# Kernel tuning notes

Hardware: AMD Instinct MI355X
Metric: run time of the kernel (lower is better)

Reference implementation:

```python
import jax, jax.numpy as jnp
import numpy as np


def _rnn_scan(x_pre, W_hh, b_hh, h0):
    # x_pre: [S, B, H] precomputed input projection; returns stacked h: [S, B, H]
    def step(h, xp):
        h = jnp.tanh(xp + h @ W_hh.T + b_hh)
        return h, h
    _, hs = jax.lax.scan(step, h0, x_pre)
    return hs


def setup_inputs() -> dict:
    key = jax.random.key(0)
    ks = jax.random.split(key, 12)
    B, S, E, H, V = 16, 256, 512, 1024, 32000
    sE, sH = 1.0 / np.sqrt(E), 1.0 / np.sqrt(H)
    return {
        "x_ids": jax.random.randint(ks[0], (B, S), 0, V),
        "emb": jax.random.normal(ks[1], (V, E), jnp.float32),
        "W_ih1": jax.random.normal(ks[2], (H, E), jnp.float32) * sE,
        "b_ih1": jax.random.normal(ks[3], (H,), jnp.float32) * sH,
        "W_hh1": jax.random.normal(ks[4], (H, H), jnp.float32) * sH,
        "b_hh1": jax.random.normal(ks[5], (H,), jnp.float32) * sH,
        "W_ih2": jax.random.normal(ks[6], (H, H), jnp.float32) * sH,
        "b_ih2": jax.random.normal(ks[7], (H,), jnp.float32) * sH,
        "W_hh2": jax.random.normal(ks[8], (H, H), jnp.float32) * sH,
        "b_hh2": jax.random.normal(ks[9], (H,), jnp.float32) * sH,
        "W_fc": jax.random.normal(ks[10], (V, H), jnp.float32) * sH,
        "b_fc": jax.random.normal(ks[11], (V,), jnp.float32) * sH,
    }


def reference(x_ids, emb, W_ih1, b_ih1, W_hh1, b_hh1, W_ih2, b_ih2, W_hh2, b_hh2, W_fc, b_fc):
    B, S = x_ids.shape
    H = W_hh1.shape[0]
    x = emb[x_ids]  # [B, S, E]
    # layer 1: precompute input projection for all steps, scan over time
    x1 = jnp.einsum('bse,he->sbh', x, W_ih1) + b_ih1  # [S, B, H]
    h0 = jnp.zeros((B, H), x.dtype)
    h1s = _rnn_scan(x1, W_hh1, b_hh1, h0)  # [S, B, H]
    # layer 2
    x2 = jnp.einsum('sbh,gh->sbg', h1s, W_ih2) + b_ih2
    h2s = _rnn_scan(x2, W_hh2, b_hh2, h0)  # [S, B, H]
    # per-step fc + softmax, vectorized
    logits = jnp.einsum('sbh,vh->bsv', h2s, W_fc) + b_fc  # [B, S, V]
    return jax.nn.softmax(logits, axis=-1)
```

## Files before the change

kernel.cpp:

```cpp
#include <hip/hip_runtime.h>
#include <cstdint>
#include <cstddef>
#include <math.h>

typedef unsigned short u16;
typedef __attribute__((ext_vector_type(4))) float f32x4;
typedef __attribute__((ext_vector_type(8))) short s16x8;
typedef __attribute__((ext_vector_type(8))) unsigned short u16x8;
typedef __attribute__((ext_vector_type(4))) unsigned short u16x4;
typedef __attribute__((ext_vector_type(4))) unsigned u32x4;

#define B_ 16
#define S_ 256
#define E_ 512
#define H_ 1024
#define V_ 32000
#define M_TOK (S_*B_)
#define BH (B_*H_)
#define NT_FC 250
#define MT_FC 32
#define NCVT 250

__device__ __forceinline__ u16 f2bf(float f) {
  union { float f; unsigned u; } x; x.f = f;
  unsigned r = x.u + 0x7fffu + ((x.u >> 16) & 1u);
  return (u16)(r >> 16);
}
__device__ __forceinline__ float bf2f(u16 x) {
  union { unsigned u; float f; } c; c.u = ((unsigned)x) << 16; return c.f;
}

__device__ __forceinline__ void sc_load16(s16x8& d, const u16* p) {
  asm volatile("global_load_dwordx4 %0, %1, off sc0 sc1" : "=v"(d) : "v"(p));
}
__device__ __forceinline__ void sc_load16u(u32x4& d, const u16* p) {
  asm volatile("global_load_dwordx4 %0, %1, off sc0 sc1" : "=v"(d) : "v"(p));
}
__device__ __forceinline__ void sc_load8w(u16x4& d, const u16* p) {
  asm volatile("global_load_dwordx2 %0, %1, off sc0 sc1\n\ts_waitcnt vmcnt(0)"
               : "=v"(d) : "v"(p) : "memory");
}
__device__ __forceinline__ int sc_load4w(const int* p) {
  int d;
  asm volatile("global_load_dword %0, %1, off sc0 sc1\n\ts_waitcnt vmcnt(0)"
               : "=v"(d) : "v"(p) : "memory");
  return d;
}
__device__ __forceinline__ void sc_store8(u16* p, u16x4 v) {
  asm volatile("global_store_dwordx2 %0, %1, off sc0 sc1" :: "v"(p), "v"(v) : "memory");
}
__device__ __forceinline__ void sc_store4(int* p, int v) {
  asm volatile("global_store_dword %0, %1, off sc0 sc1" :: "v"(p), "v"(v) : "memory");
}
__device__ __forceinline__ void wait_vm0() {
  asm volatile("s_waitcnt vmcnt(0)" ::: "memory");
}

__global__ __launch_bounds__(256)
void k_cvt_small(const float* s0, u16* d0, int n0,
                 const float* s1, u16* d1, int n1,
                 const float* s2, u16* d2, int n2,
                 const float* s3, u16* d3, int n3)
{
  const int total = n0 + n1 + n2 + n3;
  for (int i = blockIdx.x*256 + threadIdx.x; i < total; i += gridDim.x*256) {
    const float* s; u16* d; int j = i;
    if (j < n0) { s = s0; d = d0; }
    else { j -= n0;
      if (j < n1) { s = s1; d = d1; }
      else { j -= n1;
        if (j < n2) { s = s2; d = d2; }
        else { j -= n2; s = s3; d = d3; } } }
    float4 v = reinterpret_cast<const float4*>(s)[j];
    ushort4 o;
    o.x = f2bf(v.x); o.y = f2bf(v.y); o.z = f2bf(v.z); o.w = f2bf(v.w);
    reinterpret_cast<ushort4*>(d)[j] = o;
  }
}

__global__ __launch_bounds__(256) void k_embed(const int* __restrict__ ids,
                                               const float* __restrict__ emb,
                                               u16* __restrict__ A1) {
  int g = blockIdx.x*256 + threadIdx.x;
  int m = g >> 6;
  int c = g & 63;
  int s = m >> 4, b = m & 15;
  int id = ids[b*S_ + s];
  const float4* src = reinterpret_cast<const float4*>(emb + (size_t)id*E_ + (size_t)c*8);
  float4 v0 = src[0], v1 = src[1];
  u16x8 o;
  o[0]=f2bf(v0.x); o[1]=f2bf(v0.y); o[2]=f2bf(v0.z); o[3]=f2bf(v0.w);
  o[4]=f2bf(v1.x); o[5]=f2bf(v1.y); o[6]=f2bf(v1.z); o[7]=f2bf(v1.w);
  *reinterpret_cast<u16x8*>(A1 + (size_t)m*E_ + (size_t)c*8) = o;
}

#define BM 128
#define BN 128
#define BK 32

__device__ __forceinline__ void gload_lds16(const u16* g, u16* l) {
  __builtin_amdgcn_global_load_lds(
      (const __attribute__((address_space(1))) void*)g,
      (__attribute__((address_space(3))) void*)l,
      16, 0, 0);
}

template<int FCMODE>
__global__ __launch_bounds__(256)
void k_gemm(const u16* __restrict__ A, const u16* __restrict__ Bw,
            float* __restrict__ C, const float* __restrict__ bias,
            int M, int N, int K)
{
  __shared__ u16 lA[2][BM*BK];
  __shared__ u16 lB[2][BN*BK];
  const int tid = threadIdx.x;
  const int l = tid & 63, w = tid >> 6;

  const int nwg = gridDim.x * gridDim.y;
  int d = blockIdx.y * gridDim.x + blockIdx.x;
  int tt = (d & 7) * (nwg >> 3) + (d >> 3);
  const int n0 = (tt / gridDim.y) * BN;
  const int m0 = (tt % gridDim.y) * BM;

  const int wr = w >> 1, wc = w & 1;

  const int L0 = (w*2+0)*64 + l;
  const int L1 = (w*2+1)*64 + l;
  const int r0 = L0 >> 2, r1 = L1 >> 2;
  const int c0 = (L0 & 3) ^ ((r0 >> 1) & 3);
  const int c1 = (L1 & 3) ^ ((r1 >> 1) & 3);
  const u16* gA0 = A  + (size_t)(m0 + r0)*K + c0*8;
  const u16* gA1 = A  + (size_t)(m0 + r1)*K + c1*8;
  const u16* gB0 = Bw + (size_t)(n0 + r0)*K + c0*8;
  const u16* gB1 = Bw + (size_t)(n0 + r1)*K + c1*8;

  const int fr = l & 15;
  const int xc = (l >> 4) ^ ((fr >> 1) & 3);
  int aoff[4], boff[4];
#pragma unroll
  for (int f = 0; f < 4; ++f) {
    aoff[f] = (wr*64 + f*16 + fr) * BK + xc*8;
    boff[f] = (wc*64 + f*16 + fr) * BK + xc*8;
  }

  f32x4 acc[4][4] = {};
  const int KT = K / BK;

  gload_lds16(gA0, &lA[0][(w*2+0)*512]);
  gload_lds16(gA1, &lA[0][(w*2+1)*512]);
  gload_lds16(gB0, &lB[0][(w*2+0)*512]);
  gload_lds16(gB1, &lB[0][(w*2+1)*512]);
  __syncthreads();

  for (int kt = 0; kt < KT; ++kt) {
    const int buf = kt & 1;
    if (kt + 1 < KT) {
      const int koff = (kt+1)*BK;
      gload_lds16(gA0 + koff, &lA[buf^1][(w*2+0)*512]);
      gload_lds16(gA1 + koff, &lA[buf^1][(w*2+1)*512]);
      gload_lds16(gB0 + koff, &lB[buf^1][(w*2+0)*512]);
      gload_lds16(gB1 + koff, &lB[buf^1][(w*2+1)*512]);
    }
    s16x8 af[4], bq[4];
#pragma unroll
    for (int f = 0; f < 4; ++f) af[f] = *reinterpret_cast<const s16x8*>(&lA[buf][aoff[f]]);
#pragma unroll
    for (int f = 0; f < 4; ++f) bq[f] = *reinterpret_cast<const s16x8*>(&lB[buf][boff[f]]);
#pragma unroll
    for (int fm = 0; fm < 4; ++fm)
#pragma unroll
      for (int fn = 0; fn < 4; ++fn)
        acc[fm][fn] = __builtin_amdgcn_mfma_f32_16x16x32_bf16(af[fm], bq[fn], acc[fm][fn], 0, 0, 0);
    __syncthreads();
  }

  const int rowb = (l >> 4) * 4;
  const int colb = l & 15;
#pragma unroll
  for (int fm = 0; fm < 4; ++fm) {
#pragma unroll
    for (int fn = 0; fn < 4; ++fn) {
      const int col = n0 + wc*64 + fn*16 + colb;
#pragma unroll
      for (int r = 0; r < 4; ++r) {
        const int row = m0 + wr*64 + fm*16 + rowb + r;
        float v = acc[fm][fn][r];
        if (FCMODE == 2) {
          ((u16*)C)[(size_t)row*N + col] = f2bf(v);
        } else {
          C[(size_t)row*N + col] = v;
        }
      }
    }
  }
}

__device__ __forceinline__ void fc_tile(const u16* __restrict__ A, const u16* __restrict__ Bw,
                                        float* __restrict__ C, const float* __restrict__ bias,
                                        float* __restrict__ stat,
                                        int m0, int n0, u16* smem)
{
  const int tid = threadIdx.x;
  const int l = tid & 63, w = tid >> 6;
  const int wr = w >> 1, wc = w & 1;
  const int nt = n0 / BN;
  u16* lA = smem;
  u16* lB = smem + 8192;

  const int L0 = (w*2+0)*64 + l;
  const int L1 = (w*2+1)*64 + l;
  const int r0 = L0 >> 2, r1 = L1 >> 2;
  const int c0 = (L0 & 3) ^ ((r0 >> 1) & 3);
  const int c1 = (L1 & 3) ^ ((r1 >> 1) & 3);
  const u16* gA0 = A  + (size_t)(m0 + r0)*H_ + c0*8;
  const u16* gA1 = A  + (size_t)(m0 + r1)*H_ + c1*8;
  const u16* gB0 = Bw + (size_t)(n0 + r0)*H_ + c0*8;
  const u16* gB1 = Bw + (size_t)(n0 + r1)*H_ + c1*8;

  const int fr = l & 15;
  const int xc = (l >> 4) ^ ((fr >> 1) & 3);
  int aoff[4], boff[4];
#pragma unroll
  for (int f = 0; f < 4; ++f) {
    aoff[f] = (wr*64 + f*16 + fr) * BK + xc*8;
    boff[f] = (wc*64 + f*16 + fr) * BK + xc*8;
  }

  f32x4 acc[4][4] = {};

  gload_lds16(gA0, lA + (w*2+0)*512);
  gload_lds16(gA1, lA + (w*2+1)*512);
  gload_lds16(gB0, lB + (w*2+0)*512);
  gload_lds16(gB1, lB + (w*2+1)*512);
  __syncthreads();

  for (int kt = 0; kt < 32; ++kt) {
    const int buf = kt & 1;
    if (kt + 1 < 32) {
      const int koff = (kt+1)*BK;
      gload_lds16(gA0 + koff, lA + (buf^1)*4096 + (w*2+0)*512);
      gload_lds16(gA1 + koff, lA + (buf^1)*4096 + (w*2+1)*512);
      gload_lds16(gB0 + koff, lB + (buf^1)*4096 + (w*2+0)*512);
      gload_lds16(gB1 + koff, lB + (buf^1)*4096 + (w*2+1)*512);
    }
    s16x8 af[4], bq[4];
#pragma unroll
    for (int f = 0; f < 4; ++f) af[f] = *reinterpret_cast<const s16x8*>(lA + buf*4096 + aoff[f]);
#pragma unroll
    for (int f = 0; f < 4; ++f) bq[f] = *reinterpret_cast<const s16x8*>(lB + buf*4096 + boff[f]);
#pragma unroll
    for (int fm = 0; fm < 4; ++fm)
#pragma unroll
      for (int fn = 0; fn < 4; ++fn)
        acc[fm][fn] = __builtin_amdgcn_mfma_f32_16x16x32_bf16(af[fm], bq[fn], acc[fm][fn], 0, 0, 0);
    __syncthreads();
  }

  const int rowb = (l >> 4) * 4;
  const int colb = l & 15;

#pragma unroll
  for (int fm = 0; fm < 4; ++fm) {
#pragma unroll
    for (int fn = 0; fn < 4; ++fn) {
      const int col = n0 + wc*64 + fn*16 + colb;
      const float bv = bias[col];
#pragma unroll
      for (int r = 0; r < 4; ++r) {
        const int row = m0 + wr*64 + fm*16 + rowb + r;
        const int b = row & 15, s = row >> 4;
        acc[fm][fn][r] += bv;
        C[((size_t)(b*S_ + s))*V_ + col] = acc[fm][fn][r];
      }
    }
  }

  float* stats = reinterpret_cast<float*>(smem);
#pragma unroll
  for (int fm = 0; fm < 4; ++fm) {
#pragma unroll
    for (int r = 0; r < 4; ++r) {
      float sm = __expf(acc[fm][0][r]) + __expf(acc[fm][1][r])
               + __expf(acc[fm][2][r]) + __expf(acc[fm][3][r]);
#pragma unroll
      for (int o = 1; o <= 8; o <<= 1) sm += __shfl_xor(sm, o);
      if (colb == 0) {
        const int j = wr*64 + fm*16 + rowb + r;
        stats[j*2 + wc] = sm;
      }
    }
  }
  __syncthreads();
  if (tid < 128) {
    stat[(size_t)(m0 + tid)*NT_FC + nt] = stats[tid*2 + 0] + stats[tid*2 + 1];
  }
}

__global__ __launch_bounds__(256)
void k_mega(const u16* __restrict__ Whh1, const u16* __restrict__ Wih2,
            const u16* __restrict__ Whh2, const u16* __restrict__ x1b,
            const float* __restrict__ bih1, const float* __restrict__ bhh1,
            const float* __restrict__ bih2, const float* __restrict__ bhh2,
            u16* __restrict__ h1s, u16* __restrict__ u2s, u16* __restrict__ h2s,
            int* __restrict__ s1, int* __restrict__ su, int* __restrict__ s2,
            const float* __restrict__ Wfc, u16* __restrict__ Wfcb,
            const float* __restrict__ bfc,
            float* __restrict__ out, float* __restrict__ stat,
            int* __restrict__ prog2, int* __restrict__ done, int* __restrict__ cvtdone)
{
  __shared__ u16 smem[16384];
  const int bid = blockIdx.x;
  const int tid = threadIdx.x;

  if (bid < 48) {
    const int l = tid & 63, w = tid >> 6;
    const int role = bid >> 4;
    const int blk  = bid & 15;
    const int rowA = blk*64 + w*16 + (l & 15);
    const int kc = l >> 4;
    const int bcol = l & 15;
    const int i0 = blk*64 + w*16 + kc*4;
    const int jme = (tid & 127) >> 3;

    const u16* Wsel = (role == 0) ? Whh1 : (role == 1) ? Wih2 : Whh2;
    s16x8 wf[32];
    {
      const u16* wp = Wsel + (size_t)rowA*H_ + kc*8;
#pragma unroll
      for (int ks = 0; ks < 32; ++ks) wf[ks] = *reinterpret_cast<const s16x8*>(wp + ks*32);
    }

    auto stage = [&](const u16* src, const int* sentrow) {
      while (sc_load4w(sentrow + jme) != 0) __builtin_amdgcn_s_sleep(2);
      s16x8 stg[8];
#pragma unroll
      for (int r = 0; r < 8; ++r) sc_load16(stg[r], src + (size_t)(tid + r*256)*8);
      wait_vm0();
#pragma unroll
      for (int r = 0; r < 8; ++r) {
        int idx8 = tid + r*256;
        int bt = idx8 >> 7, c8 = idx8 & 127;
        *reinterpret_cast<s16x8*>(reinterpret_cast<char*>(smem) +
            bt*2048 + ((c8*16) ^ ((bt & 7) << 4))) = stg[r];
      }
    };

    const int swz = (bcol & 7) << 4;
    auto hfrag = [&](int ks) -> s16x8 {
      return *reinterpret_cast<const s16x8*>(
          reinterpret_cast<const char*>(smem) + bcol*2048 + (((kc*16) + ks*64) ^ swz));
    };
    auto mfma32 = [&](f32x4& a0, f32x4& a1, f32x4& a2, f32x4& a3) {
#pragma unroll
      for (int ks = 0; ks < 32; ks += 4) {
        a0 = __builtin_amdgcn_mfma_f32_16x16x32_bf16(wf[ks+0], hfrag(ks+0), a0, 0, 0, 0);
        a1 = __builtin_amdgcn_mfma_f32_16x16x32_bf16(wf[ks+1], hfrag(ks+1), a1, 0, 0, 0);
        a2 = __builtin_amdgcn_mfma_f32_16x16x32_bf16(wf[ks+2], hfrag(ks+2), a2, 0, 0, 0);
        a3 = __builtin_amdgcn_mfma_f32_16x16x32_bf16(wf[ks+3], hfrag(ks+3), a3, 0, 0, 0);
      }
    };

    if (role == 0) {
      float bc[4];
#pragma unroll
      for (int r = 0; r < 4; ++r) bc[r] = bih1[i0+r] + bhh1[i0+r];
      for (int t = 0; t < S_; ++t) {
        f32x4 a0 = {}, a1 = {}, a2 = {}, a3 = {};
        if (t > 0) {
          stage(h1s + (size_t)(t-1)*BH, s1 + (t-1)*16);
          __syncthreads();
          mfma32(a0, a1, a2, a3);
        }
        u16x4 xr = *reinterpret_cast<const u16x4*>(x1b + (size_t)(t*B_ + bcol)*H_ + i0);
        f32x4 tot = (a0 + a1) + (a2 + a3);
        u16x4 o;
        o[0] = f2bf(tanhf(tot[0] + bf2f(xr[0]) + bc[0]));
        o[1] = f2bf(tanhf(tot[1] + bf2f(xr[1]) + bc[1]));
        o[2] = f2bf(tanhf(tot[2] + bf2f(xr[2]) + bc[2]));
        o[3] = f2bf(tanhf(tot[3] + bf2f(xr[3]) + bc[3]));
        sc_store8(h1s + (size_t)(t*B_ + bcol)*H_ + i0, o);
        wait_vm0();
        __syncthreads();
        if (tid == 0) sc_store4(s1 + t*16 + blk, 0);
      }
    } else if (role == 1) {
      float bc[4];
#pragma unroll
      for (int r = 0; r < 4; ++r) bc[r] = bih2[i0+r] + bhh2[i0+r];
      for (int t = 0; t < S_; ++t) {
        stage(h1s + (size_t)t*BH, s1 + t*16);
        __syncthreads();
        f32x4 a0 = {}, a1 = {}, a2 = {}, a3 = {};
        mfma32(a0, a1, a2, a3);
        f32x4 tot = (a0 + a1) + (a2 + a3);
        u16x4 o;
        o[0] = f2bf(tot[0] + bc[0]);
        o[1] = f2bf(tot[1] + bc[1]);
        o[2] = f2bf(tot[2] + bc[2]);
        o[3] = f2bf(tot[3] + bc[3]);
        sc_store8(u2s + (size_t)(t*B_ + bcol)*H_ + i0, o);
        wait_vm0();
        __syncthreads();
        if (tid == 0) sc_store4(su + t*16 + blk, 0);
      }
    } else {
      for (int t = 0; t < S_; ++t) {
        if (tid == 0) {
          while (sc_load4w(su + t*16 + blk) != 0) __builtin_amdgcn_s_sleep(2);
        }
        if (t > 0) stage(h2s + (size_t)(t-1)*BH, s2 + (t-1)*16);
        __syncthreads();
        u16x4 uv;
        sc_load8w(uv, u2s + (size_t)(t*B_ + bcol)*H_ + i0);
        f32x4 a0 = {}, a1 = {}, a2 = {}, a3 = {};
        if (t > 0) mfma32(a0, a1, a2, a3);
        f32x4 tot = (a0 + a1) + (a2 + a3);
        u16x4 o;
        o[0] = f2bf(tanhf(tot[0] + bf2f(uv[0])));
        o[1] = f2bf(tanhf(tot[1] + bf2f(uv[1])));
        o[2] = f2bf(tanhf(tot[2] + bf2f(uv[2])));
        o[3] = f2bf(tanhf(tot[3] + bf2f(uv[3])));
        sc_store8(h2s + (size_t)(t*B_ + bcol)*H_ + i0, o);
        wait_vm0();
        __syncthreads();
        if (tid == 0) {
          sc_store4(s2 + t*16 + blk, 0);
          sc_store4(prog2 + blk, t + 1);
        }
      }
    }
    return;
  }

  if (bid < 48 + NCVT) {
    const int nt = bid - 48;
    const float* src = Wfc  + (size_t)nt*128*H_;
    u16*         dst = Wfcb + (size_t)nt*128*H_;
#pragma unroll 4
    for (int i = 0; i < 128; ++i) {
      const int idx = tid + i*256;
      float4 v = reinterpret_cast<const float4*>(src)[idx];
      u16x4 o;
      o[0] = f2bf(v.x); o[1] = f2bf(v.y); o[2] = f2bf(v.z); o[3] = f2bf(v.w);
      sc_store8(dst + (size_t)idx*4, o);
    }
    wait_vm0();
    __syncthreads();
    if (tid == 0) sc_store4(cvtdone + nt, 1);
    return;
  }

  const int q = bid - 48 - NCVT;
  if (q >= MT_FC * NT_FC) return;
  const int mt = q / NT_FC;
  const int nt = q - mt * NT_FC;
  const unsigned need = (unsigned)((mt + 1) * 8);

  __shared__ int s_ok;
  if (tid == 0) {
    int ok = 0;
    const u16* pp = (const u16*)prog2;
    for (int it = 0; it < 2500; ++it) {
      u32x4 pa, pb, pc, pd;
      sc_load16u(pa, pp); sc_load16u(pb, pp + 8);
      sc_load16u(pc, pp + 16); sc_load16u(pd, pp + 24);
      wait_vm0();
      unsigned m0 = pa[0] < pa[1] ? pa[0] : pa[1];
      unsigned m1 = pa[2] < pa[3] ? pa[2] : pa[3];
      unsigned m2 = pb[0] < pb[1] ? pb[0] : pb[1];
      unsigned m3 = pb[2] < pb[3] ? pb[2] : pb[3];
      unsigned m4 = pc[0] < pc[1] ? pc[0] : pc[1];
      unsigned m5 = pc[2] < pc[3] ? pc[2] : pc[3];
      unsigned m6 = pd[0] < pd[1] ? pd[0] : pd[1];
      unsigned m7 = pd[2] < pd[3] ? pd[2] : pd[3];
      m0 = m0 < m1 ? m0 : m1;  m2 = m2 < m3 ? m2 : m3;
      m4 = m4 < m5 ? m4 : m5;  m6 = m6 < m7 ? m6 : m7;
      m0 = m0 < m2 ? m0 : m2;  m4 = m4 < m6 ? m4 : m6;
      unsigned mn = m0 < m4 ? m0 : m4;
      if (mn >= need && sc_load4w(cvtdone + nt) != 0) { ok = 1; break; }
      __builtin_amdgcn_s_sleep(32);
    }
    s_ok = ok;
  }
  __syncthreads();
  if (!s_ok) return;

  fc_tile(h2s, Wfcb, out, bfc, stat, mt*BM, nt*BN, smem);
  if (tid == 0) done[q] = 1;
}

__global__ __launch_bounds__(256)
void k_fc_cleanup(const u16* __restrict__ h2s, const u16* __restrict__ Wfcb,
                  const float* __restrict__ bfc, float* __restrict__ out,
                  float* __restrict__ stat, const int* __restrict__ done)
{
  __shared__ u16 smem[16384];
  const int q = blockIdx.x;
  if (done[q]) return;
  const int mt = q / NT_FC;
  const int nt = q - mt * NT_FC;
  fc_tile(h2s, Wfcb, out, bfc, stat, mt*BM, nt*BN, smem);
}

__global__ __launch_bounds__(256)
void k_norm(float* __restrict__ out, const float* __restrict__ stat) {
  const int gw = (blockIdx.x*256 + threadIdx.x) >> 6;
  const int l = threadIdx.x & 63;
  const int b = gw & 15, s = gw >> 4;
  float* row = out + ((size_t)b*S_ + s)*V_;
  const float* st = stat + (size_t)gw*NT_FC;
  float sum = 0.f;
  for (int i = l; i < NT_FC; i += 64) sum += st[i];
#pragma unroll
  for (int o = 32; o; o >>= 1) sum += __shfl_xor(sum, o);
  const float inv = 1.f / sum;
  for (int it = 0; it < 125; ++it) {
    float4 x = reinterpret_cast<const float4*>(row)[it*64 + l];
    float4 p;
    p.x = __expf(x.x)*inv; p.y = __expf(x.y)*inv;
    p.z = __expf(x.z)*inv; p.w = __expf(x.w)*inv;
    reinterpret_cast<float4*>(row)[it*64 + l] = p;
  }
}

extern "C" void kernel_launch(void* const* d_in, const int* in_sizes, int n_in,
                              void* d_out, int out_size, void* d_ws, size_t ws_size,
                              hipStream_t stream) {
  (void)in_sizes; (void)n_in; (void)out_size; (void)ws_size;
  const int*   x_ids = (const int*)  d_in[0];
  const float* emb   = (const float*)d_in[1];
  const float* Wih1  = (const float*)d_in[2];
  const float* bih1  = (const float*)d_in[3];
  const float* Whh1  = (const float*)d_in[4];
  const float* bhh1  = (const float*)d_in[5];
  const float* Wih2  = (const float*)d_in[6];
  const float* bih2  = (const float*)d_in[7];
  const float* Whh2  = (const float*)d_in[8];
  const float* bhh2  = (const float*)d_in[9];
  const float* Wfc   = (const float*)d_in[10];
  const float* bfc   = (const float*)d_in[11];
  float* out = (float*)d_out;

  char* ws = (char*)d_ws;
  size_t off = 0;
  auto alloc = [&](size_t bytes) {
    char* p = ws + off; off += (bytes + 255) & ~(size_t)255; return p;
  };
  int* sent   = (int*) alloc(3 * S_ * 16 * 4);
  const int CTRL_INTS = 16 + MT_FC*NT_FC + NCVT;
  int* ctrl   = (int*) alloc(CTRL_INTS * 4);
  float* stat = (float*)alloc((size_t)M_TOK * NT_FC * 4);
  u16* Wfcb   = (u16*) alloc((size_t)V_*H_*2);
  u16* Whh1b  = (u16*) alloc((size_t)H_*H_*2);
  u16* Wih2b  = (u16*) alloc((size_t)H_*H_*2);
  u16* Whh2b  = (u16*) alloc((size_t)H_*H_*2);
  u16* x1b    = (u16*) alloc((size_t)M_TOK*H_*2);
  u16* h1s    = (u16*) alloc((size_t)M_TOK*H_*2);
  u16* u2s    = (u16*) alloc((size_t)M_TOK*H_*2);
  u16* h2s    = (u16*) alloc((size_t)M_TOK*H_*2);
  u16* A1     = (u16*) alloc((size_t)M_TOK*E_*2);
  u16* Wih1b  = (u16*) alloc((size_t)H_*E_*2);
  int* s1 = sent, *su = sent + S_*16, *s2 = sent + 2*S_*16;
  int* prog2   = ctrl;
  int* done    = ctrl + 16;
  int* cvtdone = done + MT_FC*NT_FC;

  k_cvt_small<<<1024, 256, 0, stream>>>(Wih1, Wih1b, H_*E_/4,
                                        Whh1, Whh1b, H_*H_/4,
                                        Wih2, Wih2b, H_*H_/4,
                                        Whh2, Whh2b, H_*H_/4);
  k_embed<<<M_TOK*64/256, 256, 0, stream>>>(x_ids, emb, A1);

  k_gemm<2><<<dim3(H_/BN, M_TOK/BM), 256, 0, stream>>>(A1, Wih1b, (float*)x1b, nullptr, M_TOK, H_, E_);

  hipMemsetAsync(sent, 0xFF, 3 * S_ * 16 * 4, stream);
  hipMemsetAsync(ctrl, 0, CTRL_INTS * 4, stream);

  k_mega<<<48 + NCVT + MT_FC*NT_FC, 256, 0, stream>>>(
      Whh1b, Wih2b, Whh2b, x1b, bih1, bhh1, bih2, bhh2,
      h1s, u2s, h2s, s1, su, s2, Wfc, Wfcb, bfc, out, stat, prog2, done, cvtdone);

  k_fc_cleanup<<<MT_FC*NT_FC, 256, 0, stream>>>(h2s, Wfcb, bfc, out, stat, done);
  k_norm<<<M_TOK/4, 256, 0, stream>>>(out, stat);
}
```

Measured before the change: 1.570 ms.

## Fuse layer-1 input projection GEMM into persistent mega kernel with per-chunk flags

Removes the separate x1 projection GEMM launch and computes its 128x128 tiles inside the mega kernel as extra blocks, each tile bumping a per-row-chunk counter. The layer-1 recurrent blocks wait on that counter every 8 timesteps, so the recurrence can start before the whole projection finishes and overlaps with it. The recurrence blocks also get raised wave priority via s_setprio. This adds spin-waiting and narrow 2-byte system-coherent stores in the tile epilogue, which may be slower per store, and relies on those x1 blocks being scheduled alongside the persistent blocks.

```diff
diff --git a/kernel.cpp b/kernel.cpp
--- a/kernel.cpp
+++ b/kernel.cpp
@@ -20,6 +20,7 @@
 #define NT_FC 250
 #define MT_FC 32
 #define NCVT 250
+#define NX1  256
 
 __device__ __forceinline__ u16 f2bf(float f) {
   union { float f; unsigned u; } x; x.f = f;
@@ -51,6 +52,9 @@
 }
 __device__ __forceinline__ void sc_store4(int* p, int v) {
   asm volatile("global_store_dword %0, %1, off sc0 sc1" :: "v"(p), "v"(v) : "memory");
+}
+__device__ __forceinline__ void sc_store2(u16* p, u16 v) {
+  asm volatile("global_store_short %0, %1, off sc0 sc1" :: "v"(p), "v"(v) : "memory");
 }
 __device__ __forceinline__ void wait_vm0() {
   asm volatile("s_waitcnt vmcnt(0)" ::: "memory");
@@ -105,34 +109,24 @@
       16, 0, 0);
 }
 
-template<int FCMODE>
-__global__ __launch_bounds__(256)
-void k_gemm(const u16* __restrict__ A, const u16* __restrict__ Bw,
-            float* __restrict__ C, const float* __restrict__ bias,
-            int M, int N, int K)
+__device__ __forceinline__ void x1_tile(const u16* __restrict__ A, const u16* __restrict__ Bw,
+                                        u16* __restrict__ Cb, int m0, int n0, u16* smem)
 {
-  __shared__ u16 lA[2][BM*BK];
-  __shared__ u16 lB[2][BN*BK];
   const int tid = threadIdx.x;
   const int l = tid & 63, w = tid >> 6;
-
-  const int nwg = gridDim.x * gridDim.y;
-  int d = blockIdx.y * gridDim.x + blockIdx.x;
-  int tt = (d & 7) * (nwg >> 3) + (d >> 3);
-  const int n0 = (tt / gridDim.y) * BN;
-  const int m0 = (tt % gridDim.y) * BM;
-
   const int wr = w >> 1, wc = w & 1;
+  u16* lA = smem;
+  u16* lB = smem + 8192;
 
   const int L0 = (w*2+0)*64 + l;
   const int L1 = (w*2+1)*64 + l;
   const int r0 = L0 >> 2, r1 = L1 >> 2;
   const int c0 = (L0 & 3) ^ ((r0 >> 1) & 3);
   const int c1 = (L1 & 3) ^ ((r1 >> 1) & 3);
-  const u16* gA0 = A  + (size_t)(m0 + r0)*K + c0*8;
-  const u16* gA1 = A  + (size_t)(m0 + r1)*K + c1*8;
-  const u16* gB0 = Bw + (size_t)(n0 + r0)*K + c0*8;
-  const u16* gB1 = Bw + (size_t)(n0 + r1)*K + c1*8;
+  const u16* gA0 = A  + (size_t)(m0 + r0)*E_ + c0*8;
+  const u16* gA1 = A  + (size_t)(m0 + r1)*E_ + c1*8;
+  const u16* gB0 = Bw + (size_t)(n0 + r0)*E_ + c0*8;
+  const u16* gB1 = Bw + (size_t)(n0 + r1)*E_ + c1*8;
 
   const int fr = l & 15;
   const int xc = (l >> 4) ^ ((fr >> 1) & 3);
@@ -144,28 +138,27 @@
   }
 
   f32x4 acc[4][4] = {};
-  const int KT = K / BK;
-
-  gload_lds16(gA0, &lA[0][(w*2+0)*512]);
-  gload_lds16(gA1, &lA[0][(w*2+1)*512]);
-  gload_lds16(gB0, &lB[0][(w*2+0)*512]);
-  gload_lds16(gB1, &lB[0][(w*2+1)*512]);
+
+  gload_lds16(gA0, lA + (w*2+0)*512);
+  gload_lds16(gA1, lA + (w*2+1)*512);
+  gload_lds16(gB0, lB + (w*2+0)*512);
+  gload_lds16(gB1, lB + (w*2+1)*512);
   __syncthreads();
 
-  for (int kt = 0; kt < KT; ++kt) {
+  for (int kt = 0; kt < 16; ++kt) {
     const int buf = kt & 1;
-    if (kt + 1 < KT) {
+    if (kt + 1 < 16) {
       const int koff = (kt+1)*BK;
-      gload_lds16(gA0 + koff, &lA[buf^1][(w*2+0)*512]);
-      gload_lds16(gA1 + koff, &lA[buf^1][(w*2+1)*512]);
-      gload_lds16(gB0 + koff, &lB[buf^1][(w*2+0)*512]);
-      gload_lds16(gB1 + koff, &lB[buf^1][(w*2+1)*512]);
+      gload_lds16(gA0 + koff, lA + (buf^1)*4096 + (w*2+0)*512);
+      gload_lds16(gA1 + koff, lA + (buf^1)*4096 + (w*2+1)*512);
+      gload_lds16(gB0 + koff, lB + (buf^1)*4096 + (w*2+0)*512);
+      gload_lds16(gB1 + koff, lB + (buf^1)*4096 + (w*2+1)*512);
     }
     s16x8 af[4], bq[4];
 #pragma unroll
-    for (int f = 0; f < 4; ++f) af[f] = *reinterpret_cast<const s16x8*>(&lA[buf][aoff[f]]);
-#pragma unroll
-    for (int f = 0; f < 4; ++f) bq[f] = *reinterpret_cast<const s16x8*>(&lB[buf][boff[f]]);
+    for (int f = 0; f < 4; ++f) af[f] = *reinterpret_cast<const s16x8*>(lA + buf*4096 + aoff[f]);
+#pragma unroll
+    for (int f = 0; f < 4; ++f) bq[f] = *reinterpret_cast<const s16x8*>(lB + buf*4096 + boff[f]);
 #pragma unroll
     for (int fm = 0; fm < 4; ++fm)
 #pragma unroll
@@ -184,12 +177,7 @@
 #pragma unroll
       for (int r = 0; r < 4; ++r) {
         const int row = m0 + wr*64 + fm*16 + rowb + r;
-        float v = acc[fm][fn][r];
-        if (FCMODE == 2) {
-          ((u16*)C)[(size_t)row*N + col] = f2bf(v);
-        } else {
-          C[(size_t)row*N + col] = v;
-        }
+        sc_store2(Cb + (size_t)row*H_ + col, f2bf(acc[fm][fn][r]));
       }
     }
   }
@@ -298,7 +286,8 @@
 
 __global__ __launch_bounds__(256)
 void k_mega(const u16* __restrict__ Whh1, const u16* __restrict__ Wih2,
-            const u16* __restrict__ Whh2, const u16* __restrict__ x1b,
+            const u16* __restrict__ Whh2, const u16* __restrict__ A1,
+            const u16* __restrict__ Wih1b, u16* __restrict__ x1b,
             const float* __restrict__ bih1, const float* __restrict__ bhh1,
             const float* __restrict__ bih2, const float* __restrict__ bhh2,
             u16* __restrict__ h1s, u16* __restrict__ u2s, u16* __restrict__ h2s,
@@ -306,13 +295,15 @@
             const float* __restrict__ Wfc, u16* __restrict__ Wfcb,
             const float* __restrict__ bfc,
             float* __restrict__ out, float* __restrict__ stat,
-            int* __restrict__ prog2, int* __restrict__ done, int* __restrict__ cvtdone)
+            int* __restrict__ prog2, int* __restrict__ done,
+            int* __restrict__ cvtdone, int* __restrict__ x1cnt)
 {
   __shared__ u16 smem[16384];
   const int bid = blockIdx.x;
   const int tid = threadIdx.x;
 
   if (bid < 48) {
+    __builtin_amdgcn_s_setprio(3);
     const int l = tid & 63, w = tid >> 6;
     const int role = bid >> 4;
     const int blk  = bid & 15;
@@ -365,6 +356,11 @@
 #pragma unroll
       for (int r = 0; r < 4; ++r) bc[r] = bih1[i0+r] + bhh1[i0+r];
       for (int t = 0; t < S_; ++t) {
+        if ((t & 7) == 0) {
+          if (tid == 0)
+            while (sc_load4w(x1cnt + (t >> 3)) < 8) __builtin_amdgcn_s_sleep(2);
+          __syncthreads();
+        }
         f32x4 a0 = {}, a1 = {}, a2 = {}, a3 = {};
         if (t > 0) {
           stage(h1s + (size_t)(t-1)*BH, s1 + (t-1)*16);
@@ -432,8 +428,19 @@
     return;
   }
 
-  if (bid < 48 + NCVT) {
-    const int nt = bid - 48;
+  if (bid < 48 + NX1) {
+    const int tt = bid - 48;
+    const int mt = tt >> 3, ntile = tt & 7;
+    x1_tile(A1, Wih1b, x1b, mt*BM, ntile*BN, smem);
+    wait_vm0();
+    __syncthreads();
+    if (tid == 0)
+      __hip_atomic_fetch_add(x1cnt + mt, 1, __ATOMIC_RELAXED, __HIP_MEMORY_SCOPE_AGENT);
+    return;
+  }
+
+  if (bid < 48 + NX1 + NCVT) {
+    const int nt = bid - 48 - NX1;
     const float* src = Wfc  + (size_t)nt*128*H_;
     u16*         dst = Wfcb + (size_t)nt*128*H_;
 #pragma unroll 4
@@ -450,7 +457,7 @@
     return;
   }
 
-  const int q = bid - 48 - NCVT;
+  const int q = bid - 48 - NX1 - NCVT;
   if (q >= MT_FC * NT_FC) return;
   const int mt = q / NT_FC;
   const int nt = q - mt * NT_FC;
@@ -547,7 +554,7 @@
     char* p = ws + off; off += (bytes + 255) & ~(size_t)255; return p;
   };
   int* sent   = (int*) alloc(3 * S_ * 16 * 4);
-  const int CTRL_INTS = 16 + MT_FC*NT_FC + NCVT;
+  const int CTRL_INTS = 16 + MT_FC*NT_FC + NCVT + 32;
   int* ctrl   = (int*) alloc(CTRL_INTS * 4);
   float* stat = (float*)alloc((size_t)M_TOK * NT_FC * 4);
   u16* Wfcb   = (u16*) alloc((size_t)V_*H_*2);
@@ -564,6 +571,7 @@
   int* prog2   = ctrl;
   int* done    = ctrl + 16;
   int* cvtdone = done + MT_FC*NT_FC;
+  int* x1cnt   = cvtdone + NCVT;
 
   k_cvt_small<<<1024, 256, 0, stream>>>(Wih1, Wih1b, H_*E_/4,
                                         Whh1, Whh1b, H_*H_/4,
@@ -571,14 +579,13 @@
                                         Whh2, Whh2b, H_*H_/4);
   k_embed<<<M_TOK*64/256, 256, 0, stream>>>(x_ids, emb, A1);
 
-  k_gemm<2><<<dim3(H_/BN, M_TOK/BM), 256, 0, stream>>>(A1, Wih1b, (float*)x1b, nullptr, M_TOK, H_, E_);
-
   hipMemsetAsync(sent, 0xFF, 3 * S_ * 16 * 4, stream);
   hipMemsetAsync(ctrl, 0, CTRL_INTS * 4, stream);
 
-  k_mega<<<48 + NCVT + MT_FC*NT_FC, 256, 0, stream>>>(
-      Whh1b, Wih2b, Whh2b, x1b, bih1, bhh1, bih2, bhh2,
-      h1s, u2s, h2s, s1, su, s2, Wfc, Wfcb, bfc, out, stat, prog2, done, cvtdone);
+  k_mega<<<48 + NX1 + NCVT + MT_FC*NT_FC, 256, 0, stream>>>(
+      Whh1b, Wih2b, Whh2b, A1, Wih1b, x1b, bih1, bhh1, bih2, bhh2,
+      h1s, u2s, h2s, s1, su, s2, Wfc, Wfcb, bfc, out, stat, prog2, done,
+      cvtdone, x1cnt);
 
   k_fc_cleanup<<<MT_FC*NT_FC, 256, 0, stream>>>(h2s, Wfcb, bfc, out, stat, done);
   k_norm<<<M_TOK/4, 256, 0, stream>>>(out, stat);
```

After: 1.556 ms (median of 2 runs). No clear change (-0.9%).
